# Kernel optimization log

Measured on AMD Instinct MI355X. Metric: run time of the kernel, lower is better.

The kernel has to match this reference:

```python
import jax, jax.numpy as jnp
import numpy as np

N, D, K, E = 100000, 256, 16, 3200000
COLLAPSE_REG = 0.1


def setup_inputs() -> dict:
    key = jax.random.key(0)
    k1, k2, k3 = jax.random.split(key, 3)
    features = jax.random.normal(k1, (N, D), dtype=jnp.float32)
    edge_index = jax.random.randint(k2, (2, E), 0, N, dtype=jnp.int32)
    adj_vals = jnp.ones((E,), dtype=jnp.float32)
    # orthogonal-ish init for linear weight, zero bias (as in nn.init.orthogonal_/zeros_)
    W = jax.random.normal(k3, (K, D), dtype=jnp.float32) / np.sqrt(D).astype(np.float32)
    b = jnp.zeros((K,), dtype=jnp.float32)
    return {"features": features, "edge_index": edge_index, "adj_vals": adj_vals, "W": W, "b": b}


def reference(features, edge_index, adj_vals, W, b):
    n = features.shape[0]
    k = W.shape[0]
    # cluster assignment: softmax(linear(features)); dropout_rate=0 -> identity
    assignments = jax.nn.softmax(features @ W.T + b, axis=-1)  # [n, k]

    rows, cols = edge_index[0], edge_index[1]
    # node degrees from sparse adjacency (row sums)
    degrees = jax.ops.segment_sum(adj_vals, rows, num_segments=n)  # [n]
    m2 = jnp.sum(degrees)  # 2m (total edge weight * 2)

    # SpMM: (A @ S) via edge-wise gather + segment-sum scatter
    AS = jax.ops.segment_sum(adj_vals[:, None] * assignments[cols], rows, num_segments=n)  # [n, k]
    graph_pooled = assignments.T @ AS  # [k, k] = S^T A S

    # modularity null-model normalizer: (S^T d)(d^T S) / 2m
    left = assignments.T @ degrees  # [k]
    normalizer = jnp.outer(left, left) / m2
    spectral_loss = -jnp.trace(graph_pooled - normalizer) / m2

    cluster_sizes = jnp.sum(assignments, axis=0)  # [k]
    collapse_loss = COLLAPSE_REG * (
        jnp.linalg.norm(cluster_sizes) / n * jnp.sqrt(jnp.float32(k)) - 1.0
    )

    # pooled cluster representations: selu((S / sizes)^T X)  -> [k, d]
    assignments_pooling = assignments / cluster_sizes  # broadcast over clusters
    features_pooled = jax.nn.selu(assignments_pooling.T @ features)
    return features_pooled, assignments, spectral_loss, collapse_loss
```

## Files before the change

kernel.cpp:

```cpp
#include <hip/hip_runtime.h>

#define N_NODES 100000
#define DIM 256
#define KC 16
#define NE 3200000
#define CHUNK 64
#define NCHUNKS ((N_NODES + CHUNK - 1) / CHUNK)

#define D0STR 1168
#define GSTR  144
#define PSTR  72
#define PLANE (16 * PSTR)

using bf16x8 = __attribute__((ext_vector_type(8))) short;
using f32x4  = __attribute__((ext_vector_type(4))) float;

__device__ __forceinline__ unsigned short f2bf(float f) {
    unsigned u = __float_as_uint(f);
    return (unsigned short)((u + 0x7fffu + ((u >> 16) & 1u)) >> 16);
}
__device__ __forceinline__ unsigned packbf(float a, float b) {
    return (unsigned)f2bf(a) | ((unsigned)f2bf(b) << 16);
}

template <bool WRITE_PACK>
__global__ __launch_bounds__(256) void k_assign_stx(const float4* __restrict__ X4,
                                                    const float4* __restrict__ W4,
                                                    const float* __restrict__ bias,
                                                    float* __restrict__ S,
                                                    unsigned* __restrict__ Sb,
                                                    float* __restrict__ cs_g,
                                                    float* __restrict__ stx) {
    __shared__ __align__(16) unsigned short Xs[16 * D0STR];
    __shared__ __align__(16) unsigned short psb[2 * 16 * PSTR];
    __shared__ float csred[4][KC];

    const int lane = threadIdx.x & 63;
    const int wv   = threadIdx.x >> 6;
    const int c    = lane & 15;
    const int quad = lane >> 4;

    bf16x8 wfrag[8];
    #pragma unroll
    for (int s = 0; s < 8; s++) {
        float4 wa = W4[c * 64 + s * 8 + quad * 2];
        float4 wb = W4[c * 64 + s * 8 + quad * 2 + 1];
        union { bf16x8 v; unsigned u[4]; } wf;
        wf.u[0] = packbf(wa.x, wa.y);
        wf.u[1] = packbf(wa.z, wa.w);
        wf.u[2] = packbf(wb.x, wb.y);
        wf.u[3] = packbf(wb.z, wb.w);
        wfrag[s] = wf.v;
    }
    const float4 b4 = ((const float4*)bias)[quad];

    f32x4 acc[4];
    #pragma unroll
    for (int t = 0; t < 4; t++) acc[t] = (f32x4){0.f, 0.f, 0.f, 0.f};
    float csr[4] = {0.f, 0.f, 0.f, 0.f};

    for (int ch = blockIdx.x; ch < NCHUNKS; ch += gridDim.x) {
        const int base = ch * CHUNK;
        __syncthreads();

        {
            const int c4  = threadIdx.x & 63;
            const int r0  = threadIdx.x >> 6;
            const int d0s = c4 >> 2;
            const int wo  = (c4 & 3) * 4;
            #pragma unroll 4
            for (int s = 0; s < 16; s++) {
                int r = r0 + 4 * s;
                int rg = base + r;
                if (rg >= N_NODES) rg = N_NODES - 1;
                float4 x = X4[(size_t)rg * 64 + c4];
                *(uint2*)&Xs[d0s * D0STR + (r >> 3) * GSTR + (r & 7) * 16 + wo] =
                    make_uint2(packbf(x.x, x.y), packbf(x.z, x.w));
            }
        }
        __syncthreads();

        f32x4 la = {0.f, 0.f, 0.f, 0.f};
        {
            const int node = wv * 16 + c;
            const int gA = node >> 3, n8 = node & 7;
            #pragma unroll
            for (int s = 0; s < 8; s++) {
                const int d0 = 2 * s + (quad >> 1);
                bf16x8 xf = *(const bf16x8*)&Xs[d0 * D0STR + gA * GSTR + n8 * 16 + (quad & 1) * 8];
                la = __builtin_amdgcn_mfma_f32_16x16x32_bf16(wfrag[s], xf, la, 0, 0, 0);
            }
        }
        float lg0 = la[0] + b4.x, lg1 = la[1] + b4.y;
        float lg2 = la[2] + b4.z, lg3 = la[3] + b4.w;
        float mx = fmaxf(fmaxf(lg0, lg1), fmaxf(lg2, lg3));
        mx = fmaxf(mx, __shfl_xor(mx, 16));
        mx = fmaxf(mx, __shfl_xor(mx, 32));
        float e0 = __expf(lg0 - mx), e1 = __expf(lg1 - mx);
        float e2 = __expf(lg2 - mx), e3 = __expf(lg3 - mx);
        float ssum = e0 + e1 + e2 + e3;
        ssum += __shfl_xor(ssum, 16);
        ssum += __shfl_xor(ssum, 32);
        float inv = 1.f / ssum;
        float pvv[4] = {e0 * inv, e1 * inv, e2 * inv, e3 * inv};

        const int nn = wv * 16 + c;
        const int nd = base + nn;
        if (nd >= N_NODES) {
            pvv[0] = pvv[1] = pvv[2] = pvv[3] = 0.f;
        } else {
            *(float4*)&S[(size_t)nd * KC + quad * 4] =
                make_float4(pvv[0], pvv[1], pvv[2], pvv[3]);
            if (WRITE_PACK) {
                unsigned q0 = __float2uint_rn(pvv[0] * 255.f);
                unsigned q1 = __float2uint_rn(pvv[1] * 255.f);
                unsigned q2 = __float2uint_rn(pvv[2] * 255.f);
                unsigned q3 = __float2uint_rn(pvv[3] * 255.f);
                Sb[(size_t)nd * 4 + quad] = q0 | (q1 << 8) | (q2 << 16) | (q3 << 24);
            }
        }
        #pragma unroll
        for (int r = 0; r < 4; r++) {
            unsigned short ph = f2bf(pvv[r]);
            float pl = pvv[r] - __uint_as_float(((unsigned)ph) << 16);
            psb[(quad * 4 + r) * PSTR + nn] = ph;
            psb[PLANE + (quad * 4 + r) * PSTR + nn] = f2bf(pl);
            csr[r] += pvv[r];
        }
        __syncthreads();

        bf16x8 afH[2], afL[2];
        #pragma unroll
        for (int ks = 0; ks < 2; ks++) {
            afH[ks] = *(const bf16x8*)&psb[c * PSTR + ks * 32 + quad * 8];
            afL[ks] = *(const bf16x8*)&psb[PLANE + c * PSTR + ks * 32 + quad * 8];
        }
        #pragma unroll
        for (int t = 0; t < 4; t++) {
            const int d0  = wv * 4 + t;
            const int dlo = c;
            union { bf16x8 v; unsigned short h[8]; } bf0, bf1;
            #pragma unroll
            for (int j = 0; j < 8; j++) {
                const int n0 = quad * 8 + j;
                bf0.h[j] = Xs[d0 * D0STR + (n0 >> 3) * GSTR + (n0 & 7) * 16 + dlo];
                const int n1 = 32 + n0;
                bf1.h[j] = Xs[d0 * D0STR + (n1 >> 3) * GSTR + (n1 & 7) * 16 + dlo];
            }
            acc[t] = __builtin_amdgcn_mfma_f32_16x16x32_bf16(afH[0], bf0.v, acc[t], 0, 0, 0);
            acc[t] = __builtin_amdgcn_mfma_f32_16x16x32_bf16(afL[0], bf0.v, acc[t], 0, 0, 0);
            acc[t] = __builtin_amdgcn_mfma_f32_16x16x32_bf16(afH[1], bf1.v, acc[t], 0, 0, 0);
            acc[t] = __builtin_amdgcn_mfma_f32_16x16x32_bf16(afL[1], bf1.v, acc[t], 0, 0, 0);
        }
    }

    #pragma unroll
    for (int t = 0; t < 4; t++) {
        #pragma unroll
        for (int r = 0; r < 4; r++)
            atomicAdd(&stx[(quad * 4 + r) * DIM + (wv * 4 + t) * 16 + c], acc[t][r]);
    }

    #pragma unroll
    for (int r = 0; r < 4; r++) {
        float v = csr[r];
        v += __shfl_xor(v, 1); v += __shfl_xor(v, 2);
        v += __shfl_xor(v, 4); v += __shfl_xor(v, 8);
        csr[r] = v;
    }
    if (c == 0) {
        #pragma unroll
        for (int r = 0; r < 4; r++) csred[wv][quad * 4 + r] = csr[r];
    }
    __syncthreads();
    if (threadIdx.x < KC) {
        int t = threadIdx.x;
        atomicAdd(&cs_g[t], csred[0][t] + csred[1][t] + csred[2][t] + csred[3][t]);
    }
}

__device__ __forceinline__ void edge_acc_u8(uint4 qr, uint4 qc, float a,
                                            float (&lf)[KC], float& m2l, float& trl) {
    union { uint4 v; unsigned w[4]; } R, C;
    R.v = qr; C.v = qc;
    float dd = 0.f;
    #pragma unroll
    for (int q = 0; q < 4; q++) {
        unsigned x = R.w[q], y = C.w[q];
        float s0 = (float)(x & 0xffu);
        float s1 = (float)((x >> 8) & 0xffu);
        float s2 = (float)((x >> 16) & 0xffu);
        float s3 = (float)(x >> 24);
        float c0 = (float)(y & 0xffu);
        float c1 = (float)((y >> 8) & 0xffu);
        float c2 = (float)((y >> 16) & 0xffu);
        float c3 = (float)(y >> 24);
        dd = fmaf(s0, c0, dd); dd = fmaf(s1, c1, dd);
        dd = fmaf(s2, c2, dd); dd = fmaf(s3, c3, dd);
        lf[4 * q + 0] = fmaf(a, s0, lf[4 * q + 0]);
        lf[4 * q + 1] = fmaf(a, s1, lf[4 * q + 1]);
        lf[4 * q + 2] = fmaf(a, s2, lf[4 * q + 2]);
        lf[4 * q + 3] = fmaf(a, s3, lf[4 * q + 3]);
    }
    m2l += a;
    trl = fmaf(a, dd, trl);
}

__global__ __launch_bounds__(256) void k_edges_u8(const int* __restrict__ rows,
                                                  const int* __restrict__ cols,
                                                  const float* __restrict__ adj,
                                                  const uint4* __restrict__ Sb4,
                                                  float* __restrict__ m2_g,
                                                  float* __restrict__ tr_g,
                                                  float* __restrict__ left_g) {
    float m2l = 0.f, trl = 0.f;
    float lf[KC];
    #pragma unroll
    for (int k = 0; k < KC; k++) lf[k] = 0.f;

    const int NU = NE / 2;
    const int stride = gridDim.x * blockDim.x;
    for (int u = blockIdx.x * blockDim.x + threadIdx.x; u < NU; u += stride) {
        int2   r2 = *(const int2*)(rows + 2 * (size_t)u);
        int2   c2 = *(const int2*)(cols + 2 * (size_t)u);
        float2 a2 = *(const float2*)(adj + 2 * (size_t)u);
        uint4 qr0 = Sb4[r2.x];
        uint4 qc0 = Sb4[c2.x];
        uint4 qr1 = Sb4[r2.y];
        uint4 qc1 = Sb4[c2.y];
        edge_acc_u8(qr0, qc0, a2.x, lf, m2l, trl);
        edge_acc_u8(qr1, qc1, a2.y, lf, m2l, trl);
    }

    trl *= (1.f / 65025.f);
    #pragma unroll
    for (int k = 0; k < KC; k++) lf[k] *= (1.f / 255.f);

    #pragma unroll
    for (int off = 32; off >= 1; off >>= 1) {
        m2l += __shfl_xor(m2l, off);
        trl += __shfl_xor(trl, off);
    }
    #pragma unroll
    for (int k = 0; k < KC; k++) {
        float v = lf[k];
        #pragma unroll
        for (int off = 32; off >= 1; off >>= 1) v += __shfl_xor(v, off);
        lf[k] = v;
    }
    __shared__ float red[4][18];
    int w = threadIdx.x >> 6;
    if ((threadIdx.x & 63) == 0) {
        red[w][0] = m2l; red[w][1] = trl;
        #pragma unroll
        for (int k = 0; k < KC; k++) red[w][2 + k] = lf[k];
    }
    __syncthreads();
    int t = threadIdx.x;
    if (t < 18) {
        float v = red[0][t] + red[1][t] + red[2][t] + red[3][t];
        float* dst = (t == 0) ? m2_g : (t == 1) ? tr_g : &left_g[t - 2];
        atomicAdd(dst, v);
    }
}

__global__ __launch_bounds__(256) void k_edges_f32(const int* __restrict__ rows,
                                                   const int* __restrict__ cols,
                                                   const float* __restrict__ adj,
                                                   const float* __restrict__ S,
                                                   float* __restrict__ m2_g,
                                                   float* __restrict__ tr_g,
                                                   float* __restrict__ left_g) {
    float m2l = 0.f, trl = 0.f;
    float lf[KC];
    #pragma unroll
    for (int k = 0; k < KC; k++) lf[k] = 0.f;

    int stride = gridDim.x * blockDim.x;
    for (int e = blockIdx.x * blockDim.x + threadIdx.x; e < NE; e += stride) {
        int r = rows[e], c = cols[e];
        float a = adj[e];
        float sv[KC], cv[KC];
        const float4* sr = (const float4*)(S + (size_t)r * KC);
        const float4* sc = (const float4*)(S + (size_t)c * KC);
        #pragma unroll
        for (int qq = 0; qq < 4; qq++) {
            float4 s4 = sr[qq], c4 = sc[qq];
            sv[4*qq]=s4.x; sv[4*qq+1]=s4.y; sv[4*qq+2]=s4.z; sv[4*qq+3]=s4.w;
            cv[4*qq]=c4.x; cv[4*qq+1]=c4.y; cv[4*qq+2]=c4.z; cv[4*qq+3]=c4.w;
        }
        float dd = 0.f;
        #pragma unroll
        for (int k = 0; k < KC; k++) {
            dd += sv[k] * cv[k];
            lf[k] += a * sv[k];
        }
        m2l += a;
        trl += a * dd;
    }

    #pragma unroll
    for (int off = 32; off >= 1; off >>= 1) {
        m2l += __shfl_xor(m2l, off);
        trl += __shfl_xor(trl, off);
    }
    #pragma unroll
    for (int k = 0; k < KC; k++) {
        float v = lf[k];
        #pragma unroll
        for (int off = 32; off >= 1; off >>= 1) v += __shfl_xor(v, off);
        lf[k] = v;
    }
    __shared__ float red[4][18];
    int w = threadIdx.x >> 6;
    if ((threadIdx.x & 63) == 0) {
        red[w][0] = m2l; red[w][1] = trl;
        #pragma unroll
        for (int k = 0; k < KC; k++) red[w][2 + k] = lf[k];
    }
    __syncthreads();
    int t = threadIdx.x;
    if (t < 18) {
        float v = red[0][t] + red[1][t] + red[2][t] + red[3][t];
        float* dst = (t == 0) ? m2_g : (t == 1) ? tr_g : &left_g[t - 2];
        atomicAdd(dst, v);
    }
}

__global__ __launch_bounds__(256) void k_final(const float* __restrict__ cs,
                                               const float* __restrict__ left,
                                               const float* __restrict__ m2p,
                                               const float* __restrict__ trp,
                                               const float* __restrict__ stx,
                                               float* __restrict__ out) {
    int t = threadIdx.x;
    #pragma unroll
    for (int k = 0; k < KC; k++) {
        float v = stx[k * DIM + t] / cs[k];
        float r = (v > 0.f) ? 1.0507009873554805f * v
                            : 1.7580993408473766f * (__expf(v) - 1.f);
        out[k * DIM + t] = r;
    }
    if (t == 0) {
        float m2 = *m2p;
        float tn = 0.f;
        #pragma unroll
        for (int k = 0; k < KC; k++) tn += left[k] * left[k];
        tn /= m2;
        float spectral = -((*trp) - tn) / m2;
        float ss = 0.f;
        #pragma unroll
        for (int k = 0; k < KC; k++) ss += cs[k] * cs[k];
        float collapse = 0.1f * (sqrtf(ss) / (float)N_NODES * 4.0f - 1.0f);
        out[KC * DIM + (size_t)N_NODES * KC]     = spectral;
        out[KC * DIM + (size_t)N_NODES * KC + 1] = collapse;
    }
}

extern "C" void kernel_launch(void* const* d_in, const int* in_sizes, int n_in,
                              void* d_out, int out_size, void* d_ws, size_t ws_size,
                              hipStream_t stream) {
    (void)out_size;

    const float* X    = nullptr;
    const int*   ei   = nullptr;
    const float* adj  = nullptr;
    const float* W    = nullptr;
    const float* bias = nullptr;
    for (int i = 0; i < n_in; i++) {
        switch (in_sizes[i]) {
            case 25600000: X    = (const float*)d_in[i]; break;
            case  6400000: ei   = (const int*)d_in[i];   break;
            case  3200000: adj  = (const float*)d_in[i]; break;
            case     4096: W    = (const float*)d_in[i]; break;
            case       16: bias = (const float*)d_in[i]; break;
        }
    }

    float* out = (float*)d_out;
    float* S   = out + KC * DIM;
    const int* rows = ei;
    const int* cols = ei + NE;

    float* ws   = (float*)d_ws;
    float* cs   = ws;
    float* left = ws + 16;
    float* m2   = ws + 32;
    float* tr   = ws + 33;
    float* stx  = ws + 64;
    unsigned* Sb = (unsigned*)(ws + 64 + KC * DIM);
    const size_t need = (64 + KC * DIM) * sizeof(float) + (size_t)N_NODES * 16;
    const bool use_pack = (ws_size >= need);

    hipMemsetAsync(d_ws, 0, (64 + KC * DIM) * sizeof(float), stream);

    const int agrid = 782;
    if (use_pack) {
        k_assign_stx<true><<<agrid, 256, 0, stream>>>(
            (const float4*)X, (const float4*)W, bias, S, Sb, cs, stx);
        k_edges_u8<<<2048, 256, 0, stream>>>(rows, cols, adj, (const uint4*)Sb,
                                             m2, tr, left);
    } else {
        k_assign_stx<false><<<agrid, 256, 0, stream>>>(
            (const float4*)X, (const float4*)W, bias, S, Sb, cs, stx);
        k_edges_f32<<<2048, 256, 0, stream>>>(rows, cols, adj, S, m2, tr, left);
    }
    k_final<<<1, 256, 0, stream>>>(cs, left, m2, tr, stx, out);
}
```

Measured before the change: 248.7 us.

## Use one block per chunk, drop bf16 low plane, widen edge loads to four

The assignment kernel drops its grid-stride chunk loop and launches one block per 64-node chunk, with launch bounds set for four blocks per CU. The X loads are split into two register-staged halves interleaved with W fragment setup. The hi/lo bf16 split of the assignment probabilities is removed, so the S^T X pooling uses a single bf16 MFMA plane, halving that MFMA work at some cost in precision. The edge kernel now processes four edges per thread iteration with int4/float4 loads to raise memory-level parallelism. The trade-off is more per-block atomics to stx (1563 blocks instead of 782).

Result: no change. 248.0 us (-0.3%).

```diff
diff --git a/kernel.cpp b/kernel.cpp
--- a/kernel.cpp
+++ b/kernel.cpp
@@ -10,7 +10,6 @@
 #define D0STR 1168
 #define GSTR  144
 #define PSTR  72
-#define PLANE (16 * PSTR)
 
 using bf16x8 = __attribute__((ext_vector_type(8))) short;
 using f32x4  = __attribute__((ext_vector_type(4))) float;
@@ -24,15 +23,15 @@
 }
 
 template <bool WRITE_PACK>
-__global__ __launch_bounds__(256) void k_assign_stx(const float4* __restrict__ X4,
-                                                    const float4* __restrict__ W4,
-                                                    const float* __restrict__ bias,
-                                                    float* __restrict__ S,
-                                                    unsigned* __restrict__ Sb,
-                                                    float* __restrict__ cs_g,
-                                                    float* __restrict__ stx) {
+__global__ __launch_bounds__(256, 4) void k_assign_stx(const float4* __restrict__ X4,
+                                                       const float4* __restrict__ W4,
+                                                       const float* __restrict__ bias,
+                                                       float* __restrict__ S,
+                                                       unsigned* __restrict__ Sb,
+                                                       float* __restrict__ cs_g,
+                                                       float* __restrict__ stx) {
     __shared__ __align__(16) unsigned short Xs[16 * D0STR];
-    __shared__ __align__(16) unsigned short psb[2 * 16 * PSTR];
+    __shared__ __align__(16) unsigned short psb[16 * PSTR];
     __shared__ float csred[4][KC];
 
     const int lane = threadIdx.x & 63;
@@ -40,9 +39,23 @@
     const int c    = lane & 15;
     const int quad = lane >> 4;
 
+    const int base = blockIdx.x * CHUNK;
+
+    const int c4  = threadIdx.x & 63;
+    const int r0  = threadIdx.x >> 6;
+    const int d0s = c4 >> 2;
+    const int wo  = (c4 & 3) * 4;
+
+    float4 xr[8];
+    #pragma unroll
+    for (int s = 0; s < 8; s++) {
+        int rg = base + r0 + 4 * s;
+        if (rg >= N_NODES) rg = N_NODES - 1;
+        xr[s] = X4[(size_t)rg * 64 + c4];
+    }
     bf16x8 wfrag[8];
     #pragma unroll
-    for (int s = 0; s < 8; s++) {
+    for (int s = 0; s < 4; s++) {
         float4 wa = W4[c * 64 + s * 8 + quad * 2];
         float4 wb = W4[c * 64 + s * 8 + quad * 2 + 1];
         union { bf16x8 v; unsigned u[4]; } wf;
@@ -52,106 +65,105 @@
         wf.u[3] = packbf(wb.z, wb.w);
         wfrag[s] = wf.v;
     }
+    #pragma unroll
+    for (int s = 0; s < 8; s++) {
+        int r = r0 + 4 * s;
+        *(uint2*)&Xs[d0s * D0STR + (r >> 3) * GSTR + (r & 7) * 16 + wo] =
+            make_uint2(packbf(xr[s].x, xr[s].y), packbf(xr[s].z, xr[s].w));
+    }
+    #pragma unroll
+    for (int s = 0; s < 8; s++) {
+        int rg = base + r0 + 4 * (s + 8);
+        if (rg >= N_NODES) rg = N_NODES - 1;
+        xr[s] = X4[(size_t)rg * 64 + c4];
+    }
+    #pragma unroll
+    for (int s = 4; s < 8; s++) {
+        float4 wa = W4[c * 64 + s * 8 + quad * 2];
+        float4 wb = W4[c * 64 + s * 8 + quad * 2 + 1];
+        union { bf16x8 v; unsigned u[4]; } wf;
+        wf.u[0] = packbf(wa.x, wa.y);
+        wf.u[1] = packbf(wa.z, wa.w);
+        wf.u[2] = packbf(wb.x, wb.y);
+        wf.u[3] = packbf(wb.z, wb.w);
+        wfrag[s] = wf.v;
+    }
+    #pragma unroll
+    for (int s = 0; s < 8; s++) {
+        int r = r0 + 4 * (s + 8);
+        *(uint2*)&Xs[d0s * D0STR + (r >> 3) * GSTR + (r & 7) * 16 + wo] =
+            make_uint2(packbf(xr[s].x, xr[s].y), packbf(xr[s].z, xr[s].w));
+    }
     const float4 b4 = ((const float4*)bias)[quad];
+    __syncthreads();
+
+    f32x4 la = {0.f, 0.f, 0.f, 0.f};
+    {
+        const int node = wv * 16 + c;
+        const int gA = node >> 3, n8 = node & 7;
+        #pragma unroll
+        for (int s = 0; s < 8; s++) {
+            const int d0 = 2 * s + (quad >> 1);
+            bf16x8 xf = *(const bf16x8*)&Xs[d0 * D0STR + gA * GSTR + n8 * 16 + (quad & 1) * 8];
+            la = __builtin_amdgcn_mfma_f32_16x16x32_bf16(wfrag[s], xf, la, 0, 0, 0);
+        }
+    }
+    float lg0 = la[0] + b4.x, lg1 = la[1] + b4.y;
+    float lg2 = la[2] + b4.z, lg3 = la[3] + b4.w;
+    float mx = fmaxf(fmaxf(lg0, lg1), fmaxf(lg2, lg3));
+    mx = fmaxf(mx, __shfl_xor(mx, 16));
+    mx = fmaxf(mx, __shfl_xor(mx, 32));
+    float e0 = __expf(lg0 - mx), e1 = __expf(lg1 - mx);
+    float e2 = __expf(lg2 - mx), e3 = __expf(lg3 - mx);
+    float ssum = e0 + e1 + e2 + e3;
+    ssum += __shfl_xor(ssum, 16);
+    ssum += __shfl_xor(ssum, 32);
+    float inv = 1.f / ssum;
+    float pvv[4] = {e0 * inv, e1 * inv, e2 * inv, e3 * inv};
+
+    const int nn = wv * 16 + c;
+    const int nd = base + nn;
+    if (nd >= N_NODES) {
+        pvv[0] = pvv[1] = pvv[2] = pvv[3] = 0.f;
+    } else {
+        *(float4*)&S[(size_t)nd * KC + quad * 4] =
+            make_float4(pvv[0], pvv[1], pvv[2], pvv[3]);
+        if (WRITE_PACK) {
+            unsigned q0 = __float2uint_rn(pvv[0] * 255.f);
+            unsigned q1 = __float2uint_rn(pvv[1] * 255.f);
+            unsigned q2 = __float2uint_rn(pvv[2] * 255.f);
+            unsigned q3 = __float2uint_rn(pvv[3] * 255.f);
+            Sb[(size_t)nd * 4 + quad] = q0 | (q1 << 8) | (q2 << 16) | (q3 << 24);
+        }
+    }
+    float csr[4];
+    #pragma unroll
+    for (int r = 0; r < 4; r++) {
+        psb[(quad * 4 + r) * PSTR + nn] = f2bf(pvv[r]);
+        csr[r] = pvv[r];
+    }
+    __syncthreads();
 
     f32x4 acc[4];
     #pragma unroll
     for (int t = 0; t < 4; t++) acc[t] = (f32x4){0.f, 0.f, 0.f, 0.f};
-    float csr[4] = {0.f, 0.f, 0.f, 0.f};
-
-    for (int ch = blockIdx.x; ch < NCHUNKS; ch += gridDim.x) {
-        const int base = ch * CHUNK;
-        __syncthreads();
-
-        {
-            const int c4  = threadIdx.x & 63;
-            const int r0  = threadIdx.x >> 6;
-            const int d0s = c4 >> 2;
-            const int wo  = (c4 & 3) * 4;
-            #pragma unroll 4
-            for (int s = 0; s < 16; s++) {
-                int r = r0 + 4 * s;
-                int rg = base + r;
-                if (rg >= N_NODES) rg = N_NODES - 1;
-                float4 x = X4[(size_t)rg * 64 + c4];
-                *(uint2*)&Xs[d0s * D0STR + (r >> 3) * GSTR + (r & 7) * 16 + wo] =
-                    make_uint2(packbf(x.x, x.y), packbf(x.z, x.w));
-            }
-        }
-        __syncthreads();
-
-        f32x4 la = {0.f, 0.f, 0.f, 0.f};
-        {
-            const int node = wv * 16 + c;
-            const int gA = node >> 3, n8 = node & 7;
-            #pragma unroll
-            for (int s = 0; s < 8; s++) {
-                const int d0 = 2 * s + (quad >> 1);
-                bf16x8 xf = *(const bf16x8*)&Xs[d0 * D0STR + gA * GSTR + n8 * 16 + (quad & 1) * 8];
-                la = __builtin_amdgcn_mfma_f32_16x16x32_bf16(wfrag[s], xf, la, 0, 0, 0);
-            }
-        }
-        float lg0 = la[0] + b4.x, lg1 = la[1] + b4.y;
-        float lg2 = la[2] + b4.z, lg3 = la[3] + b4.w;
-        float mx = fmaxf(fmaxf(lg0, lg1), fmaxf(lg2, lg3));
-        mx = fmaxf(mx, __shfl_xor(mx, 16));
-        mx = fmaxf(mx, __shfl_xor(mx, 32));
-        float e0 = __expf(lg0 - mx), e1 = __expf(lg1 - mx);
-        float e2 = __expf(lg2 - mx), e3 = __expf(lg3 - mx);
-        float ssum = e0 + e1 + e2 + e3;
-        ssum += __shfl_xor(ssum, 16);
-        ssum += __shfl_xor(ssum, 32);
-        float inv = 1.f / ssum;
-        float pvv[4] = {e0 * inv, e1 * inv, e2 * inv, e3 * inv};
-
-        const int nn = wv * 16 + c;
-        const int nd = base + nn;
-        if (nd >= N_NODES) {
-            pvv[0] = pvv[1] = pvv[2] = pvv[3] = 0.f;
-        } else {
-            *(float4*)&S[(size_t)nd * KC + quad * 4] =
-                make_float4(pvv[0], pvv[1], pvv[2], pvv[3]);
-            if (WRITE_PACK) {
-                unsigned q0 = __float2uint_rn(pvv[0] * 255.f);
-                unsigned q1 = __float2uint_rn(pvv[1] * 255.f);
-                unsigned q2 = __float2uint_rn(pvv[2] * 255.f);
-                unsigned q3 = __float2uint_rn(pvv[3] * 255.f);
-                Sb[(size_t)nd * 4 + quad] = q0 | (q1 << 8) | (q2 << 16) | (q3 << 24);
-            }
-        }
-        #pragma unroll
-        for (int r = 0; r < 4; r++) {
-            unsigned short ph = f2bf(pvv[r]);
-            float pl = pvv[r] - __uint_as_float(((unsigned)ph) << 16);
-            psb[(quad * 4 + r) * PSTR + nn] = ph;
-            psb[PLANE + (quad * 4 + r) * PSTR + nn] = f2bf(pl);
-            csr[r] += pvv[r];
-        }
-        __syncthreads();
-
-        bf16x8 afH[2], afL[2];
-        #pragma unroll
-        for (int ks = 0; ks < 2; ks++) {
-            afH[ks] = *(const bf16x8*)&psb[c * PSTR + ks * 32 + quad * 8];
-            afL[ks] = *(const bf16x8*)&psb[PLANE + c * PSTR + ks * 32 + quad * 8];
-        }
-        #pragma unroll
-        for (int t = 0; t < 4; t++) {
-            const int d0  = wv * 4 + t;
-            const int dlo = c;
-            union { bf16x8 v; unsigned short h[8]; } bf0, bf1;
-            #pragma unroll
-            for (int j = 0; j < 8; j++) {
-                const int n0 = quad * 8 + j;
-                bf0.h[j] = Xs[d0 * D0STR + (n0 >> 3) * GSTR + (n0 & 7) * 16 + dlo];
-                const int n1 = 32 + n0;
-                bf1.h[j] = Xs[d0 * D0STR + (n1 >> 3) * GSTR + (n1 & 7) * 16 + dlo];
-            }
-            acc[t] = __builtin_amdgcn_mfma_f32_16x16x32_bf16(afH[0], bf0.v, acc[t], 0, 0, 0);
-            acc[t] = __builtin_amdgcn_mfma_f32_16x16x32_bf16(afL[0], bf0.v, acc[t], 0, 0, 0);
-            acc[t] = __builtin_amdgcn_mfma_f32_16x16x32_bf16(afH[1], bf1.v, acc[t], 0, 0, 0);
-            acc[t] = __builtin_amdgcn_mfma_f32_16x16x32_bf16(afL[1], bf1.v, acc[t], 0, 0, 0);
-        }
+    bf16x8 afH[2];
+    afH[0] = *(const bf16x8*)&psb[c * PSTR + 0 * 32 + quad * 8];
+    afH[1] = *(const bf16x8*)&psb[c * PSTR + 1 * 32 + quad * 8];
+    #pragma unroll
+    for (int t = 0; t < 4; t++) {
+        const int d0  = wv * 4 + t;
+        const int dlo = c;
+        union { bf16x8 v; unsigned short h[8]; } bf0, bf1;
+        #pragma unroll
+        for (int j = 0; j < 8; j++) {
+            const int n0 = quad * 8 + j;
+            bf0.h[j] = Xs[d0 * D0STR + (n0 >> 3) * GSTR + (n0 & 7) * 16 + dlo];
+            const int n1 = 32 + n0;
+            bf1.h[j] = Xs[d0 * D0STR + (n1 >> 3) * GSTR + (n1 & 7) * 16 + dlo];
+        }
+        acc[t] = __builtin_amdgcn_mfma_f32_16x16x32_bf16(afH[0], bf0.v, acc[t], 0, 0, 0);
+        acc[t] = __builtin_amdgcn_mfma_f32_16x16x32_bf16(afH[1], bf1.v, acc[t], 0, 0, 0);
     }
 
     #pragma unroll
@@ -218,18 +230,24 @@
     #pragma unroll
     for (int k = 0; k < KC; k++) lf[k] = 0.f;
 
-    const int NU = NE / 2;
+    const int NU = NE / 4;
     const int stride = gridDim.x * blockDim.x;
     for (int u = blockIdx.x * blockDim.x + threadIdx.x; u < NU; u += stride) {
-        int2   r2 = *(const int2*)(rows + 2 * (size_t)u);
-        int2   c2 = *(const int2*)(cols + 2 * (size_t)u);
-        float2 a2 = *(const float2*)(adj + 2 * (size_t)u);
-        uint4 qr0 = Sb4[r2.x];
-        uint4 qc0 = Sb4[c2.x];
-        uint4 qr1 = Sb4[r2.y];
-        uint4 qc1 = Sb4[c2.y];
-        edge_acc_u8(qr0, qc0, a2.x, lf, m2l, trl);
-        edge_acc_u8(qr1, qc1, a2.y, lf, m2l, trl);
+        int4   r4 = *(const int4*)(rows + 4 * (size_t)u);
+        int4   c4 = *(const int4*)(cols + 4 * (size_t)u);
+        float4 a4 = *(const float4*)(adj + 4 * (size_t)u);
+        uint4 qr0 = Sb4[r4.x];
+        uint4 qc0 = Sb4[c4.x];
+        uint4 qr1 = Sb4[r4.y];
+        uint4 qc1 = Sb4[c4.y];
+        uint4 qr2 = Sb4[r4.z];
+        uint4 qc2 = Sb4[c4.z];
+        uint4 qr3 = Sb4[r4.w];
+        uint4 qc3 = Sb4[c4.w];
+        edge_acc_u8(qr0, qc0, a4.x, lf, m2l, trl);
+        edge_acc_u8(qr1, qc1, a4.y, lf, m2l, trl);
+        edge_acc_u8(qr2, qc2, a4.z, lf, m2l, trl);
+        edge_acc_u8(qr3, qc3, a4.w, lf, m2l, trl);
     }
 
     trl *= (1.f / 65025.f);
@@ -394,14 +412,13 @@
 
     hipMemsetAsync(d_ws, 0, (64 + KC * DIM) * sizeof(float), stream);
 
-    const int agrid = 782;
     if (use_pack) {
-        k_assign_stx<true><<<agrid, 256, 0, stream>>>(
+        k_assign_stx<true><<<NCHUNKS, 256, 0, stream>>>(
             (const float4*)X, (const float4*)W, bias, S, Sb, cs, stx);
         k_edges_u8<<<2048, 256, 0, stream>>>(rows, cols, adj, (const uint4*)Sb,
                                              m2, tr, left);
     } else {
-        k_assign_stx<false><<<agrid, 256, 0, stream>>>(
+        k_assign_stx<false><<<NCHUNKS, 256, 0, stream>>>(
             (const float4*)X, (const float4*)W, bias, S, Sb, cs, stx);
         k_edges_f32<<<2048, 256, 0, stream>>>(rows, cols, adj, S, m2, tr, left);
     }
```

## Process one chunk per block with register-prefetched rows and single-plane bf16 pooling

Applied to the files above, without the earlier changes.

Replaces the grid-stride chunk loop in the assignment/pooling kernel with one 64-node chunk per block. The grid becomes NCHUNKS blocks and launch bounds now request 4 blocks per CU. Each wave loads all 16 of its feature rows into registers before packing them to LDS, to raise memory-level parallelism. It also drops the hi/lo split bf16 representation of S, halving the MFMA work for S^T X at the cost of precision in the pooled features. The trade-off is roughly twice as many global atomicAdds into stx, one set per block, and less per-block amortisation of the W fragment setup.

Measured after the change: 244.4 us. About the same (-1.7%).

```diff
diff --git a/kernel.cpp b/kernel.cpp
--- a/kernel.cpp
+++ b/kernel.cpp
@@ -10,7 +10,6 @@
 #define D0STR 1168
 #define GSTR  144
 #define PSTR  72
-#define PLANE (16 * PSTR)
 
 using bf16x8 = __attribute__((ext_vector_type(8))) short;
 using f32x4  = __attribute__((ext_vector_type(4))) float;
@@ -24,21 +23,23 @@
 }
 
 template <bool WRITE_PACK>
-__global__ __launch_bounds__(256) void k_assign_stx(const float4* __restrict__ X4,
-                                                    const float4* __restrict__ W4,
-                                                    const float* __restrict__ bias,
-                                                    float* __restrict__ S,
-                                                    unsigned* __restrict__ Sb,
-                                                    float* __restrict__ cs_g,
-                                                    float* __restrict__ stx) {
+__global__ __launch_bounds__(256, 4) void k_assign_stx(const float4* __restrict__ X4,
+                                                       const float4* __restrict__ W4,
+                                                       const float* __restrict__ bias,
+                                                       float* __restrict__ S,
+                                                       unsigned* __restrict__ Sb,
+                                                       float* __restrict__ cs_g,
+                                                       float* __restrict__ stx) {
     __shared__ __align__(16) unsigned short Xs[16 * D0STR];
-    __shared__ __align__(16) unsigned short psb[2 * 16 * PSTR];
+    __shared__ __align__(16) unsigned short psb[16 * PSTR];
     __shared__ float csred[4][KC];
 
     const int lane = threadIdx.x & 63;
     const int wv   = threadIdx.x >> 6;
     const int c    = lane & 15;
     const int quad = lane >> 4;
+
+    const int base = blockIdx.x * CHUNK;
 
     bf16x8 wfrag[8];
     #pragma unroll
@@ -54,104 +55,90 @@
     }
     const float4 b4 = ((const float4*)bias)[quad];
 
+    const int c4 = lane;
+    const int d0s = c4 >> 2;
+    const int wo  = (c4 & 3) * 4;
+    float4 xr[16];
+    #pragma unroll
+    for (int s = 0; s < 16; s++) {
+        int rg = base + wv * 16 + s;
+        if (rg >= N_NODES) rg = N_NODES - 1;
+        xr[s] = X4[(size_t)rg * 64 + c4];
+    }
+    #pragma unroll
+    for (int s = 0; s < 16; s++) {
+        int r = wv * 16 + s;
+        *(uint2*)&Xs[d0s * D0STR + (r >> 3) * GSTR + (r & 7) * 16 + wo] =
+            make_uint2(packbf(xr[s].x, xr[s].y), packbf(xr[s].z, xr[s].w));
+    }
+
+    f32x4 la = {0.f, 0.f, 0.f, 0.f};
+    {
+        const int node = wv * 16 + c;
+        const int gA = node >> 3, n8 = node & 7;
+        #pragma unroll
+        for (int s = 0; s < 8; s++) {
+            const int d0 = 2 * s + (quad >> 1);
+            bf16x8 xf = *(const bf16x8*)&Xs[d0 * D0STR + gA * GSTR + n8 * 16 + (quad & 1) * 8];
+            la = __builtin_amdgcn_mfma_f32_16x16x32_bf16(wfrag[s], xf, la, 0, 0, 0);
+        }
+    }
+    float lg0 = la[0] + b4.x, lg1 = la[1] + b4.y;
+    float lg2 = la[2] + b4.z, lg3 = la[3] + b4.w;
+    float mx = fmaxf(fmaxf(lg0, lg1), fmaxf(lg2, lg3));
+    mx = fmaxf(mx, __shfl_xor(mx, 16));
+    mx = fmaxf(mx, __shfl_xor(mx, 32));
+    float e0 = __expf(lg0 - mx), e1 = __expf(lg1 - mx);
+    float e2 = __expf(lg2 - mx), e3 = __expf(lg3 - mx);
+    float ssum = e0 + e1 + e2 + e3;
+    ssum += __shfl_xor(ssum, 16);
+    ssum += __shfl_xor(ssum, 32);
+    float inv = 1.f / ssum;
+    float pvv[4] = {e0 * inv, e1 * inv, e2 * inv, e3 * inv};
+
+    const int nn = wv * 16 + c;
+    const int nd = base + nn;
+    if (nd >= N_NODES) {
+        pvv[0] = pvv[1] = pvv[2] = pvv[3] = 0.f;
+    } else {
+        *(float4*)&S[(size_t)nd * KC + quad * 4] =
+            make_float4(pvv[0], pvv[1], pvv[2], pvv[3]);
+        if (WRITE_PACK) {
+            unsigned q0 = __float2uint_rn(pvv[0] * 255.f);
+            unsigned q1 = __float2uint_rn(pvv[1] * 255.f);
+            unsigned q2 = __float2uint_rn(pvv[2] * 255.f);
+            unsigned q3 = __float2uint_rn(pvv[3] * 255.f);
+            Sb[(size_t)nd * 4 + quad] = q0 | (q1 << 8) | (q2 << 16) | (q3 << 24);
+        }
+    }
+    float csr[4];
+    #pragma unroll
+    for (int r = 0; r < 4; r++) {
+        psb[(quad * 4 + r) * PSTR + nn] = f2bf(pvv[r]);
+        csr[r] = pvv[r];
+    }
+    __syncthreads();
+
     f32x4 acc[4];
     #pragma unroll
     for (int t = 0; t < 4; t++) acc[t] = (f32x4){0.f, 0.f, 0.f, 0.f};
-    float csr[4] = {0.f, 0.f, 0.f, 0.f};
-
-    for (int ch = blockIdx.x; ch < NCHUNKS; ch += gridDim.x) {
-        const int base = ch * CHUNK;
-        __syncthreads();
-
-        {
-            const int c4  = threadIdx.x & 63;
-            const int r0  = threadIdx.x >> 6;
-            const int d0s = c4 >> 2;
-            const int wo  = (c4 & 3) * 4;
-            #pragma unroll 4
-            for (int s = 0; s < 16; s++) {
-                int r = r0 + 4 * s;
-                int rg = base + r;
-                if (rg >= N_NODES) rg = N_NODES - 1;
-                float4 x = X4[(size_t)rg * 64 + c4];
-                *(uint2*)&Xs[d0s * D0STR + (r >> 3) * GSTR + (r & 7) * 16 + wo] =
-                    make_uint2(packbf(x.x, x.y), packbf(x.z, x.w));
-            }
-        }
-        __syncthreads();
-
-        f32x4 la = {0.f, 0.f, 0.f, 0.f};
-        {
-            const int node = wv * 16 + c;
-            const int gA = node >> 3, n8 = node & 7;
-            #pragma unroll
-            for (int s = 0; s < 8; s++) {
-                const int d0 = 2 * s + (quad >> 1);
-                bf16x8 xf = *(const bf16x8*)&Xs[d0 * D0STR + gA * GSTR + n8 * 16 + (quad & 1) * 8];
-                la = __builtin_amdgcn_mfma_f32_16x16x32_bf16(wfrag[s], xf, la, 0, 0, 0);
-            }
-        }
-        float lg0 = la[0] + b4.x, lg1 = la[1] + b4.y;
-        float lg2 = la[2] + b4.z, lg3 = la[3] + b4.w;
-        float mx = fmaxf(fmaxf(lg0, lg1), fmaxf(lg2, lg3));
-        mx = fmaxf(mx, __shfl_xor(mx, 16));
-        mx = fmaxf(mx, __shfl_xor(mx, 32));
-        float e0 = __expf(lg0 - mx), e1 = __expf(lg1 - mx);
-        float e2 = __expf(lg2 - mx), e3 = __expf(lg3 - mx);
-        float ssum = e0 + e1 + e2 + e3;
-        ssum += __shfl_xor(ssum, 16);
-        ssum += __shfl_xor(ssum, 32);
-        float inv = 1.f / ssum;
-        float pvv[4] = {e0 * inv, e1 * inv, e2 * inv, e3 * inv};
-
-        const int nn = wv * 16 + c;
-        const int nd = base + nn;
-        if (nd >= N_NODES) {
-            pvv[0] = pvv[1] = pvv[2] = pvv[3] = 0.f;
-        } else {
-            *(float4*)&S[(size_t)nd * KC + quad * 4] =
-                make_float4(pvv[0], pvv[1], pvv[2], pvv[3]);
-            if (WRITE_PACK) {
-                unsigned q0 = __float2uint_rn(pvv[0] * 255.f);
-                unsigned q1 = __float2uint_rn(pvv[1] * 255.f);
-                unsigned q2 = __float2uint_rn(pvv[2] * 255.f);
-                unsigned q3 = __float2uint_rn(pvv[3] * 255.f);
-                Sb[(size_t)nd * 4 + quad] = q0 | (q1 << 8) | (q2 << 16) | (q3 << 24);
-            }
-        }
-        #pragma unroll
-        for (int r = 0; r < 4; r++) {
-            unsigned short ph = f2bf(pvv[r]);
-            float pl = pvv[r] - __uint_as_float(((unsigned)ph) << 16);
-            psb[(quad * 4 + r) * PSTR + nn] = ph;
-            psb[PLANE + (quad * 4 + r) * PSTR + nn] = f2bf(pl);
-            csr[r] += pvv[r];
-        }
-        __syncthreads();
-
-        bf16x8 afH[2], afL[2];
-        #pragma unroll
-        for (int ks = 0; ks < 2; ks++) {
-            afH[ks] = *(const bf16x8*)&psb[c * PSTR + ks * 32 + quad * 8];
-            afL[ks] = *(const bf16x8*)&psb[PLANE + c * PSTR + ks * 32 + quad * 8];
-        }
-        #pragma unroll
-        for (int t = 0; t < 4; t++) {
-            const int d0  = wv * 4 + t;
-            const int dlo = c;
-            union { bf16x8 v; unsigned short h[8]; } bf0, bf1;
-            #pragma unroll
-            for (int j = 0; j < 8; j++) {
-                const int n0 = quad * 8 + j;
-                bf0.h[j] = Xs[d0 * D0STR + (n0 >> 3) * GSTR + (n0 & 7) * 16 + dlo];
-                const int n1 = 32 + n0;
-                bf1.h[j] = Xs[d0 * D0STR + (n1 >> 3) * GSTR + (n1 & 7) * 16 + dlo];
-            }
-            acc[t] = __builtin_amdgcn_mfma_f32_16x16x32_bf16(afH[0], bf0.v, acc[t], 0, 0, 0);
-            acc[t] = __builtin_amdgcn_mfma_f32_16x16x32_bf16(afL[0], bf0.v, acc[t], 0, 0, 0);
-            acc[t] = __builtin_amdgcn_mfma_f32_16x16x32_bf16(afH[1], bf1.v, acc[t], 0, 0, 0);
-            acc[t] = __builtin_amdgcn_mfma_f32_16x16x32_bf16(afL[1], bf1.v, acc[t], 0, 0, 0);
-        }
+    bf16x8 afH[2];
+    afH[0] = *(const bf16x8*)&psb[c * PSTR + 0 * 32 + quad * 8];
+    afH[1] = *(const bf16x8*)&psb[c * PSTR + 1 * 32 + quad * 8];
+    #pragma unroll
+    for (int t = 0; t < 4; t++) {
+        const int d0  = wv * 4 + t;
+        const int dlo = c;
+        union { bf16x8 v; unsigned short h[8]; } bf0, bf1;
+        #pragma unroll
+        for (int j = 0; j < 8; j++) {
+            const int n0 = quad * 8 + j;
+            bf0.h[j] = Xs[d0 * D0STR + (n0 >> 3) * GSTR + (n0 & 7) * 16 + dlo];
+            const int n1 = 32 + n0;
+            bf1.h[j] = Xs[d0 * D0STR + (n1 >> 3) * GSTR + (n1 & 7) * 16 + dlo];
+        }
+        acc[t] = __builtin_amdgcn_mfma_f32_16x16x32_bf16(afH[0], bf0.v, acc[t], 0, 0, 0);
+        acc[t] = __builtin_amdgcn_mfma_f32_16x16x32_bf16(afH[1], bf1.v, acc[t], 0, 0, 0);
     }
 
     #pragma unroll
@@ -161,16 +148,17 @@
             atomicAdd(&stx[(quad * 4 + r) * DIM + (wv * 4 + t) * 16 + c], acc[t][r]);
     }
 
+    float csr2[4];
     #pragma unroll
     for (int r = 0; r < 4; r++) {
         float v = csr[r];
         v += __shfl_xor(v, 1); v += __shfl_xor(v, 2);
         v += __shfl_xor(v, 4); v += __shfl_xor(v, 8);
-        csr[r] = v;
+        csr2[r] = v;
     }
     if (c == 0) {
         #pragma unroll
-        for (int r = 0; r < 4; r++) csred[wv][quad * 4 + r] = csr[r];
+        for (int r = 0; r < 4; r++) csred[wv][quad * 4 + r] = csr2[r];
     }
     __syncthreads();
     if (threadIdx.x < KC) {
@@ -394,14 +382,13 @@
 
     hipMemsetAsync(d_ws, 0, (64 + KC * DIM) * sizeof(float), stream);
 
-    const int agrid = 782;
     if (use_pack) {
-        k_assign_stx<true><<<agrid, 256, 0, stream>>>(
+        k_assign_stx<true><<<NCHUNKS, 256, 0, stream>>>(
             (const float4*)X, (const float4*)W, bias, S, Sb, cs, stx);
         k_edges_u8<<<2048, 256, 0, stream>>>(rows, cols, adj, (const uint4*)Sb,
                                              m2, tr, left);
     } else {
-        k_assign_stx<false><<<agrid, 256, 0, stream>>>(
+        k_assign_stx<false><<<NCHUNKS, 256, 0, stream>>>(
             (const float4*)X, (const float4*)W, bias, S, Sb, cs, stx);
         k_edges_f32<<<2048, 256, 0, stream>>>(rows, cols, adj, S, m2, tr, left);
     }
```
